# Performance work log

Hardware: AMD Instinct MI355X
Metric: run time of the kernel (lower is better)

## Reference

```python
import jax, jax.numpy as jnp
import numpy as np

NUM_ITERS = 3


def squash(s, axis=-1):
    # v = (|s|^2 / (1+|s|^2)) * s / |s|
    sq = jnp.sum(s * s, axis=axis, keepdims=True)
    return sq / (1.0 + sq) * s / jnp.sqrt(sq)


def setup_inputs() -> dict:
    key = jax.random.key(0)
    k1, k2 = jax.random.split(key)
    B, C, R, I, O = 256, 10, 1152, 8, 16
    x = jax.random.normal(k1, (B, R, I), dtype=jnp.float32)
    route_weights = jax.random.normal(k2, (C, R, I, O), dtype=jnp.float32)
    return {"x": x, "route_weights": route_weights}


def reference(x, route_weights):
    # x: [B, R, I]; route_weights: [C, R, I, O]
    # u: predictions from each route node for each output capsule: [B, C, R, 1, O]
    u = jnp.einsum("bri,crio->bcro", x, route_weights)[:, :, :, None, :]
    b = jnp.zeros_like(u)
    v = None
    for i in range(NUM_ITERS):
        c = jax.nn.softmax(b, axis=2)          # softmax over route nodes (dim=2)
        s = jnp.sum(c * u, axis=2, keepdims=True)  # [B, C, 1, 1, O]
        v = squash(s, axis=-1)
        if i != NUM_ITERS - 1:
            b = b + jnp.sum(u * v, axis=-1, keepdims=True)  # agreement, broadcast over O
    return v  # [B, C, 1, 1, O]
```

## Files before the change

### kernel.cpp

```cpp
#include <hip/hip_runtime.h>


#define B_ 256
#define C_ 10
#define R_ 1152
#define I_ 8
#define O_ 16
#define T_ 512
#define RPP 128
#define KPT 9
#define NW 8
#define NITER 3

__global__ __launch_bounds__(T_, 4) void capsule_routing_kernel(
    const float* __restrict__ x,
    const float* __restrict__ w,
    float* __restrict__ out)
{
    const int bc   = blockIdx.x;
    const int c    = bc >> 8;
    const int b    = bc & 255;
    const int tid  = threadIdx.x;
    const int lane = tid & 63;
    const int wid  = tid >> 6;
    const int oq   = tid & 3;
    const int rl   = tid >> 2;

    __shared__ float sred[NW][4][4];
    __shared__ float zred[NW];
    __shared__ float vfin[O_];

    float u[KPT][4];
    float logit[KPT];

    #pragma unroll
    for (int k = 0; k < KPT; ++k) {
        const int r = k * RPP + rl;
        const float4* xp = (const float4*)(x + ((size_t)b * R_ + r) * I_);
        const float4 xa = xp[0];
        const float4 xb = xp[1];
        const float xs[8] = {xa.x, xa.y, xa.z, xa.w, xb.x, xb.y, xb.z, xb.w};
        const float* wp = w + ((size_t)c * R_ + r) * (I_ * O_) + oq * 4;
        float4 acc = make_float4(0.f, 0.f, 0.f, 0.f);
        #pragma unroll
        for (int i = 0; i < I_; ++i) {
            const float4 wv = *(const float4*)(wp + i * O_);
            acc.x += xs[i] * wv.x;
            acc.y += xs[i] * wv.y;
            acc.z += xs[i] * wv.z;
            acc.w += xs[i] * wv.w;
        }
        u[k][0] = acc.x; u[k][1] = acc.y; u[k][2] = acc.z; u[k][3] = acc.w;
        logit[k] = 0.f;
    }

    for (int it = 0; it < NITER; ++it) {
        float zpart = 0.f, s0 = 0.f, s1 = 0.f, s2 = 0.f, s3 = 0.f;
        #pragma unroll
        for (int k = 0; k < KPT; ++k) {
            const float ek = __expf(logit[k]);
            zpart += ek;
            s0 += ek * u[k][0];
            s1 += ek * u[k][1];
            s2 += ek * u[k][2];
            s3 += ek * u[k][3];
        }
        #pragma unroll
        for (int off = 4; off <= 32; off <<= 1) {
            zpart += __shfl_xor(zpart, off);
            s0 += __shfl_xor(s0, off);
            s1 += __shfl_xor(s1, off);
            s2 += __shfl_xor(s2, off);
            s3 += __shfl_xor(s3, off);
        }
        if (lane < 4) {
            sred[wid][lane][0] = s0;
            sred[wid][lane][1] = s1;
            sred[wid][lane][2] = s2;
            sred[wid][lane][3] = s3;
            if (lane == 0) zred[wid] = zpart;
        }
        __syncthreads();

        if (wid == 0 && lane < O_) {
            float S = 0.f, Z = 0.f;
            #pragma unroll
            for (int wv = 0; wv < NW; ++wv) {
                S += sred[wv][lane >> 2][lane & 3];
                Z += zred[wv];
            }
            float p = S * S;
            p += __shfl_xor(p, 1);
            p += __shfl_xor(p, 2);
            p += __shfl_xor(p, 4);
            p += __shfl_xor(p, 8);
            const float inv = 1.f / Z;
            const float svn = S * inv;
            const float sqn = p * inv * inv;
            const float scale = sqrtf(sqn) / (1.f + sqn);
            const float vf = svn * scale;
            vfin[lane] = vf;
            if (it == NITER - 1)
                out[((size_t)b * C_ + c) * O_ + lane] = vf;
        }

        if (it != NITER - 1) {
            __syncthreads();
            const float4 vq = *(const float4*)&vfin[oq * 4];
            #pragma unroll
            for (int k = 0; k < KPT; ++k) {
                float dp = u[k][0] * vq.x + u[k][1] * vq.y +
                           u[k][2] * vq.z + u[k][3] * vq.w;
                dp += __shfl_xor(dp, 1);
                dp += __shfl_xor(dp, 2);
                logit[k] += dp;
            }
        }
    }
}

extern "C" void kernel_launch(void* const* d_in, const int* in_sizes, int n_in,
                              void* d_out, int out_size, void* d_ws, size_t ws_size,
                              hipStream_t stream) {
    const float* x = (const float*)d_in[0];
    const float* w = (const float*)d_in[1];
    float* out = (float*)d_out;
    capsule_routing_kernel<<<dim3(B_ * C_), dim3(T_), 0, stream>>>(x, w, out);
}
```

Before: 75.01 us.

## Process two batch elements per block to reuse route weight loads

Each block now handles two batch items for one output capsule, so every route-weight float4 loaded from global memory feeds two sets of FMAs. This halves the block count and the total weight traffic, which matters because the weights (about 5.9 MB) are re-read once per batch item. In exchange, per-thread register use roughly doubles (two u arrays and two logit arrays), which may reduce occupancy under the launch-bounds hint of 4 blocks, and the grid has fewer blocks to spread across CUs.

New measurement: 71.26 us. 5.0% less time.

```diff
diff --git a/kernel.cpp b/kernel.cpp
--- a/kernel.cpp
+++ b/kernel.cpp
@@ -7,6 +7,7 @@
 #define I_ 8
 #define O_ 16
 #define T_ 512
+#define BPB 2
 #define RPP 128
 #define KPT 9
 #define NW 8
@@ -17,77 +18,90 @@
     const float* __restrict__ w,
     float* __restrict__ out)
 {
-    const int bc   = blockIdx.x;
-    const int c    = bc >> 8;
-    const int b    = bc & 255;
+    const int c    = blockIdx.x >> 7;
+    const int bh   = blockIdx.x & 127;
+    const int b0   = bh * BPB;
     const int tid  = threadIdx.x;
     const int lane = tid & 63;
     const int wid  = tid >> 6;
     const int oq   = tid & 3;
     const int rl   = tid >> 2;
 
-    __shared__ float sred[NW][4][4];
-    __shared__ float zred[NW];
-    __shared__ float vfin[O_];
+    __shared__ float sred[BPB][NW][4][4];
+    __shared__ float zred[BPB][NW];
+    __shared__ float vfin[BPB][O_];
 
-    float u[KPT][4];
-    float logit[KPT];
+    float u0[KPT][4], u1[KPT][4];
+    float lg0[KPT], lg1[KPT];
 
     #pragma unroll
     for (int k = 0; k < KPT; ++k) {
         const int r = k * RPP + rl;
-        const float4* xp = (const float4*)(x + ((size_t)b * R_ + r) * I_);
-        const float4 xa = xp[0];
-        const float4 xb = xp[1];
-        const float xs[8] = {xa.x, xa.y, xa.z, xa.w, xb.x, xb.y, xb.z, xb.w};
+        const float4* xp0 = (const float4*)(x + ((size_t)b0 * R_ + r) * I_);
+        const float4 xa0 = xp0[0];
+        const float4 xb0 = xp0[1];
+        const float4* xp1 = (const float4*)(x + ((size_t)(b0 + 1) * R_ + r) * I_);
+        const float4 xa1 = xp1[0];
+        const float4 xb1 = xp1[1];
+        const float xs0[8] = {xa0.x, xa0.y, xa0.z, xa0.w, xb0.x, xb0.y, xb0.z, xb0.w};
+        const float xs1[8] = {xa1.x, xa1.y, xa1.z, xa1.w, xb1.x, xb1.y, xb1.z, xb1.w};
         const float* wp = w + ((size_t)c * R_ + r) * (I_ * O_) + oq * 4;
-        float4 acc = make_float4(0.f, 0.f, 0.f, 0.f);
+        float4 a0 = make_float4(0.f, 0.f, 0.f, 0.f);
+        float4 a1 = make_float4(0.f, 0.f, 0.f, 0.f);
         #pragma unroll
         for (int i = 0; i < I_; ++i) {
             const float4 wv = *(const float4*)(wp + i * O_);
-            acc.x += xs[i] * wv.x;
-            acc.y += xs[i] * wv.y;
-            acc.z += xs[i] * wv.z;
-            acc.w += xs[i] * wv.w;
+            a0.x += xs0[i] * wv.x;  a1.x += xs1[i] * wv.x;
+            a0.y += xs0[i] * wv.y;  a1.y += xs1[i] * wv.y;
+            a0.z += xs0[i] * wv.z;  a1.z += xs1[i] * wv.z;
+            a0.w += xs0[i] * wv.w;  a1.w += xs1[i] * wv.w;
         }
-        u[k][0] = acc.x; u[k][1] = acc.y; u[k][2] = acc.z; u[k][3] = acc.w;
-        logit[k] = 0.f;
+        u0[k][0] = a0.x; u0[k][1] = a0.y; u0[k][2] = a0.z; u0[k][3] = a0.w;
+        u1[k][0] = a1.x; u1[k][1] = a1.y; u1[k][2] = a1.z; u1[k][3] = a1.w;
+        lg0[k] = 0.f;
+        lg1[k] = 0.f;
     }
 
     for (int it = 0; it < NITER; ++it) {
-        float zpart = 0.f, s0 = 0.f, s1 = 0.f, s2 = 0.f, s3 = 0.f;
+        float z0 = 0.f, z1 = 0.f;
+        float s00 = 0.f, s01 = 0.f, s02 = 0.f, s03 = 0.f;
+        float s10 = 0.f, s11 = 0.f, s12 = 0.f, s13 = 0.f;
         #pragma unroll
         for (int k = 0; k < KPT; ++k) {
-            const float ek = __expf(logit[k]);
-            zpart += ek;
-            s0 += ek * u[k][0];
-            s1 += ek * u[k][1];
-            s2 += ek * u[k][2];
-            s3 += ek * u[k][3];
+            const float e0 = __expf(lg0[k]);
+            z0 += e0;
+            s00 += e0 * u0[k][0]; s01 += e0 * u0[k][1];
+            s02 += e0 * u0[k][2]; s03 += e0 * u0[k][3];
+            const float e1 = __expf(lg1[k]);
+            z1 += e1;
+            s10 += e1 * u1[k][0]; s11 += e1 * u1[k][1];
+            s12 += e1 * u1[k][2]; s13 += e1 * u1[k][3];
         }
         #pragma unroll
         for (int off = 4; off <= 32; off <<= 1) {
-            zpart += __shfl_xor(zpart, off);
-            s0 += __shfl_xor(s0, off);
-            s1 += __shfl_xor(s1, off);
-            s2 += __shfl_xor(s2, off);
-            s3 += __shfl_xor(s3, off);
+            z0 += __shfl_xor(z0, off);   z1 += __shfl_xor(z1, off);
+            s00 += __shfl_xor(s00, off); s01 += __shfl_xor(s01, off);
+            s02 += __shfl_xor(s02, off); s03 += __shfl_xor(s03, off);
+            s10 += __shfl_xor(s10, off); s11 += __shfl_xor(s11, off);
+            s12 += __shfl_xor(s12, off); s13 += __shfl_xor(s13, off);
         }
         if (lane < 4) {
-            sred[wid][lane][0] = s0;
-            sred[wid][lane][1] = s1;
-            sred[wid][lane][2] = s2;
-            sred[wid][lane][3] = s3;
-            if (lane == 0) zred[wid] = zpart;
+            sred[0][wid][lane][0] = s00; sred[0][wid][lane][1] = s01;
+            sred[0][wid][lane][2] = s02; sred[0][wid][lane][3] = s03;
+            sred[1][wid][lane][0] = s10; sred[1][wid][lane][1] = s11;
+            sred[1][wid][lane][2] = s12; sred[1][wid][lane][3] = s13;
+            if (lane == 0) { zred[0][wid] = z0; zred[1][wid] = z1; }
         }
         __syncthreads();
 
-        if (wid == 0 && lane < O_) {
+        if (wid == 0 && lane < 2 * O_) {
+            const int bb = lane >> 4;
+            const int o  = lane & 15;
             float S = 0.f, Z = 0.f;
             #pragma unroll
             for (int wv = 0; wv < NW; ++wv) {
-                S += sred[wv][lane >> 2][lane & 3];
-                Z += zred[wv];
+                S += sred[bb][wv][o >> 2][o & 3];
+                Z += zred[bb][wv];
             }
             float p = S * S;
             p += __shfl_xor(p, 1);
@@ -99,21 +113,27 @@
             const float sqn = p * inv * inv;
             const float scale = sqrtf(sqn) / (1.f + sqn);
             const float vf = svn * scale;
-            vfin[lane] = vf;
+            vfin[bb][o] = vf;
             if (it == NITER - 1)
-                out[((size_t)b * C_ + c) * O_ + lane] = vf;
+                out[((size_t)(b0 + bb) * C_ + c) * O_ + o] = vf;
         }
 
         if (it != NITER - 1) {
             __syncthreads();
-            const float4 vq = *(const float4*)&vfin[oq * 4];
+            const float4 v0 = *(const float4*)&vfin[0][oq * 4];
+            const float4 v1 = *(const float4*)&vfin[1][oq * 4];
             #pragma unroll
             for (int k = 0; k < KPT; ++k) {
-                float dp = u[k][0] * vq.x + u[k][1] * vq.y +
-                           u[k][2] * vq.z + u[k][3] * vq.w;
-                dp += __shfl_xor(dp, 1);
-                dp += __shfl_xor(dp, 2);
-                logit[k] += dp;
+                float d0 = u0[k][0] * v0.x + u0[k][1] * v0.y +
+                           u0[k][2] * v0.z + u0[k][3] * v0.w;
+                float d1 = u1[k][0] * v1.x + u1[k][1] * v1.y +
+                           u1[k][2] * v1.z + u1[k][3] * v1.w;
+                d0 += __shfl_xor(d0, 1);
+                d0 += __shfl_xor(d0, 2);
+                d1 += __shfl_xor(d1, 1);
+                d1 += __shfl_xor(d1, 2);
+                lg0[k] += d0;
+                lg1[k] += d1;
             }
         }
     }
@@ -125,5 +145,5 @@
     const float* x = (const float*)d_in[0];
     const float* w = (const float*)d_in[1];
     float* out = (float*)d_out;
-    capsule_routing_kernel<<<dim3(B_ * C_), dim3(T_), 0, stream>>>(x, w, out);
+    capsule_routing_kernel<<<dim3(C_ * (B_ / BPB)), dim3(T_), 0, stream>>>(x, w, out);
 }
```
